# Kernel optimization log

Hardware: AMD Instinct MI355X
Metric: run time of the kernel (lower is better)

Reference implementation:

```python
import jax, jax.numpy as jnp
import numpy as np

ALPHA = 0.1
EPS = 1e-10

def setup_inputs() -> dict:
    key = jax.random.key(0)
    k1, k2 = jax.random.split(key)
    x = jax.random.normal(k1, (64, 8192, 128), dtype=jnp.float32)   # [B, N, D]
    pv = jax.random.uniform(k2, (64, 128), dtype=jnp.float32)        # [M, D] prototypes (torch.rand init)
    return {"x": x, "pv": pv}

def _cdist(x, pv):
    # Euclidean pairwise distance via GEMM form: [B,N,D] x [M,D] -> [B,N,M]
    x2 = jnp.sum(x * x, axis=-1, keepdims=True)          # [B,N,1]
    p2 = jnp.sum(pv * pv, axis=-1)                        # [M]
    xp = jnp.einsum('bnd,md->bnm', x, pv)                 # [B,N,M]
    return jnp.sqrt(jnp.maximum(x2 + p2 - 2.0 * xp, 0.0))

def reference(x, pv):
    dist = _cdist(x, pv)                                  # [B,N,M]
    min_dist = jnp.min(dist, axis=1)                      # [B,M] closest patch per prototype
    min_pos = jnp.argmin(dist, axis=1)                    # [B,M]
    # pick, per batch, the patch position of the globally closest prototype (no-grad in original)
    idx = jnp.argmin(min_dist, axis=1)                    # [B]
    min_pos = min_pos[jnp.arange(min_pos.shape[0]), idx]  # [B]
    max_sim = jnp.exp(EPS - ALPHA * min_dist)             # [B,M]
    return (max_sim, min_pos)
```

## Files before the change

### kernel.cpp

```cpp
#include <hip/hip_runtime.h>
#include <cfloat>
#include <cmath>

#define B_ 64
#define N_ 8192
#define D_ 128
#define M_ 64
#define CROWS 64
#define NCHUNK 4
#define BROWS (CROWS*NCHUNK)
#define NBLK (N_/BROWS)
#define ALPHA_ 0.1f
#define EPS_ 1e-10f

typedef __attribute__((ext_vector_type(4))) float f32x4;
typedef __attribute__((ext_vector_type(8))) short bf16x8;
typedef __attribute__((ext_vector_type(4))) short s16x4;

static __device__ __forceinline__ short f2bf(float f) {
    unsigned u = __float_as_uint(f);
    u += 0x7fff + ((u >> 16) & 1);
    return (short)(u >> 16);
}
static __device__ __forceinline__ float bf2f(short s) {
    return __uint_as_float(((unsigned)(unsigned short)s) << 16);
}

__global__ __launch_bounds__(256, 2)
void protomin_mfma(const float* __restrict__ x, const float* __restrict__ pv,
                   float* __restrict__ wsv, int* __restrict__ wsa) {
    __shared__ short xhi[2][CROWS * D_];
    __shared__ short xlo[2][CROWS * D_];
    __shared__ float x2s[2][CROWS];
    __shared__ float redv[4][M_];
    __shared__ int   redp[4][M_];

    const int tid = threadIdx.x;
    const int w   = tid >> 6;
    const int l   = tid & 63;
    const int lm  = l & 15, lg = l >> 4;
    const int bid = blockIdx.x;
    const int b   = bid >> 5;
    const int nbase = (bid & 31) * BROWS;

    const float* xblk = x + ((size_t)b * N_ + nbase) * D_;

    f32x4 nv[8];
    {
        const f32x4* src = (const f32x4*)xblk;
#pragma unroll
        for (int i = 0; i < 8; ++i) nv[i] = src[(w * 8 + i) * 64 + l];
    }

    bf16x8 Bh[4][4], Bl[4][4];
#pragma unroll
    for (int mt = 0; mt < 4; ++mt) {
#pragma unroll
        for (int kt = 0; kt < 4; ++kt) {
            const float* p = pv + (mt * 16 + lm) * D_ + kt * 32 + lg * 8;
            f32x4 p0 = *(const f32x4*)p;
            f32x4 p1 = *(const f32x4*)(p + 4);
#pragma unroll
            for (int j = 0; j < 4; ++j) {
                short h = f2bf(p0[j]);
                Bh[mt][kt][j] = h;
                Bl[mt][kt][j] = f2bf(p0[j] - bf2f(h));
            }
#pragma unroll
            for (int j = 0; j < 4; ++j) {
                short h = f2bf(p1[j]);
                Bh[mt][kt][4 + j] = h;
                Bl[mt][kt][4 + j] = f2bf(p1[j] - bf2f(h));
            }
        }
    }

    auto stage = [&](int buf) {
#pragma unroll
        for (int i = 0; i < 8; ++i) {
            int seg = w * 8 + i;
            int row = seg * 2 + (l >> 5);
            int ks  = (l & 31) * 4;
            f32x4 v = nv[i];
            float s = v[0] * v[0];
            s = fmaf(v[1], v[1], s); s = fmaf(v[2], v[2], s); s = fmaf(v[3], v[3], s);
            s += __shfl_xor(s, 1);  s += __shfl_xor(s, 2);  s += __shfl_xor(s, 4);
            s += __shfl_xor(s, 8);  s += __shfl_xor(s, 16);
            if ((l & 31) == 0) x2s[buf][row] = s;
            s16x4 hv, lv;
#pragma unroll
            for (int j = 0; j < 4; ++j) {
                short h = f2bf(v[j]);
                hv[j] = h;
                lv[j] = f2bf(v[j] - bf2f(h));
            }
            int sidx = row * D_ + (ks ^ ((row & 7) << 3));
            *(s16x4*)&xhi[buf][sidx] = hv;
            *(s16x4*)&xlo[buf][sidx] = lv;
        }
    };

    float bv[4]; int bp[4];
#pragma unroll
    for (int mt = 0; mt < 4; ++mt) { bv[mt] = FLT_MAX; bp[mt] = 0; }

    stage(0);
    __syncthreads();

    for (int c = 0; c < NCHUNK; ++c) {
        const int cur = c & 1;
        if (c + 1 < NCHUNK) {
            const f32x4* src = (const f32x4*)(xblk + (size_t)(c + 1) * CROWS * D_);
#pragma unroll
            for (int i = 0; i < 8; ++i) nv[i] = src[(w * 8 + i) * 64 + l];
        }

        f32x4 acc[4] = {};
        const int arow  = w * 16 + lm;
        const int abase = arow * D_;
        const int aswz  = (arow & 7) << 3;
#pragma unroll
        for (int kt = 0; kt < 4; ++kt) {
            int koff = (kt * 32 + lg * 8) ^ aswz;
            bf16x8 ah = *(const bf16x8*)&xhi[cur][abase + koff];
            bf16x8 al = *(const bf16x8*)&xlo[cur][abase + koff];
#pragma unroll
            for (int mt = 0; mt < 4; ++mt) {
                acc[mt] = __builtin_amdgcn_mfma_f32_16x16x32_bf16(ah, Bh[mt][kt], acc[mt], 0, 0, 0);
                acc[mt] = __builtin_amdgcn_mfma_f32_16x16x32_bf16(al, Bh[mt][kt], acc[mt], 0, 0, 0);
                acc[mt] = __builtin_amdgcn_mfma_f32_16x16x32_bf16(ah, Bl[mt][kt], acc[mt], 0, 0, 0);
                acc[mt] = __builtin_amdgcn_mfma_f32_16x16x32_bf16(al, Bl[mt][kt], acc[mt], 0, 0, 0);
            }
        }

        float x2v[4];
        const int rbase = w * 16 + lg * 4;
#pragma unroll
        for (int r = 0; r < 4; ++r) x2v[r] = x2s[cur][rbase + r];
        const int npos0 = nbase + c * CROWS + rbase;
#pragma unroll
        for (int mt = 0; mt < 4; ++mt) {
#pragma unroll
            for (int r = 0; r < 4; ++r) {
                float cand = fmaf(-2.f, acc[mt][r], x2v[r]);
                if (cand < bv[mt]) { bv[mt] = cand; bp[mt] = npos0 + r; }
            }
        }

        if (c + 1 < NCHUNK) stage(cur ^ 1);
        __syncthreads();
    }

#pragma unroll
    for (int mt = 0; mt < 4; ++mt) {
        float v = bv[mt]; int p = bp[mt];
#pragma unroll
        for (int off = 16; off <= 32; off <<= 1) {
            float ov = __shfl_xor(v, off);
            int   op = __shfl_xor(p, off);
            if (ov < v || (ov == v && op < p)) { v = ov; p = op; }
        }
        if (l < 16) { redv[w][mt * 16 + l] = v; redp[w][mt * 16 + l] = p; }
    }
    __syncthreads();

    if (tid < M_) {
        float v = redv[0][tid]; int p = redp[0][tid];
#pragma unroll
        for (int w2 = 1; w2 < 4; ++w2) {
            float ov = redv[w2][tid]; int op = redp[w2][tid];
            if (ov < v || (ov == v && op < p)) { v = ov; p = op; }
        }
        wsv[(size_t)bid * M_ + tid] = v;
        wsa[(size_t)bid * M_ + tid] = p;
    }
}

__global__ void finalize_kernel(const float* __restrict__ wsv,
                                const int* __restrict__ wsa,
                                const float* __restrict__ pv,
                                float* __restrict__ out) {
    const int b = blockIdx.x;
    const int m = threadIdx.x;

    float p2 = 0.f;
    const f32x4* pp = (const f32x4*)(pv + m * D_);
#pragma unroll 8
    for (int j = 0; j < 32; ++j) {
        f32x4 v = pp[j];
        p2 = fmaf(v[0], v[0], p2); p2 = fmaf(v[1], v[1], p2);
        p2 = fmaf(v[2], v[2], p2); p2 = fmaf(v[3], v[3], p2);
    }

    float v = FLT_MAX; int p = 0;
    for (int bc = 0; bc < NBLK; ++bc) {
        size_t idx = ((size_t)(b * NBLK + bc)) * M_ + m;
        float nv2 = wsv[idx]; int np = wsa[idx];
        if (nv2 < v || (nv2 == v && np < p)) { v = nv2; p = np; }
    }
    float dist = sqrtf(fmaxf(v + p2, 0.f));
    out[b * M_ + m] = expf(EPS_ - ALPHA_ * dist);

    __shared__ float sv[M_];
    __shared__ int   sa[M_];
    sv[m] = dist; sa[m] = p;
    __syncthreads();
    if (m == 0) {
        float best = FLT_MAX; int bpos = 0;
        for (int k = 0; k < M_; ++k)
            if (sv[k] < best) { best = sv[k]; bpos = sa[k]; }
        out[B_ * M_ + b] = (float)bpos;
    }
}

extern "C" void kernel_launch(void* const* d_in, const int* in_sizes, int n_in,
                              void* d_out, int out_size, void* d_ws, size_t ws_size,
                              hipStream_t stream) {
    const float* x  = (const float*)d_in[0];
    const float* pv = (const float*)d_in[1];
    float* out = (float*)d_out;

    float* wsv = (float*)d_ws;
    int*   wsa = (int*)((char*)d_ws + (size_t)B_ * NBLK * M_ * sizeof(float));

    hipLaunchKernelGGL(protomin_mfma, dim3(B_ * NBLK), dim3(256), 0, stream,
                       x, pv, wsv, wsa);
    hipLaunchKernelGGL(finalize_kernel, dim3(B_), dim3(M_), 0, stream,
                       wsv, wsa, pv, out);
}
```

Baseline: 449.5 us.

## Split warps into a 2x2 row/prototype tile grid to halve B-fragment registers

Each wave now owns 32 rows by 32 prototypes instead of 16 rows by 64 prototypes. The bf16 hi/lo prototype fragments held in registers drop by half, which cuts register pressure and may allow more occupancy. In exchange each wave loads twice as many A fragments from LDS per k-step. The cross-wave reduction is reduced to combining two row halves.

```diff
diff --git a/kernel.cpp b/kernel.cpp
--- a/kernel.cpp
+++ b/kernel.cpp
@@ -32,13 +32,15 @@
     __shared__ short xhi[2][CROWS * D_];
     __shared__ short xlo[2][CROWS * D_];
     __shared__ float x2s[2][CROWS];
-    __shared__ float redv[4][M_];
-    __shared__ int   redp[4][M_];
+    __shared__ float redv[2][M_];
+    __shared__ int   redp[2][M_];
 
     const int tid = threadIdx.x;
     const int w   = tid >> 6;
     const int l   = tid & 63;
     const int lm  = l & 15, lg = l >> 4;
+    const int wr  = w & 1;
+    const int wm  = w >> 1;
     const int bid = blockIdx.x;
     const int b   = bid >> 5;
     const int nbase = (bid & 31) * BROWS;
@@ -52,25 +54,25 @@
         for (int i = 0; i < 8; ++i) nv[i] = src[(w * 8 + i) * 64 + l];
     }
 
-    bf16x8 Bh[4][4], Bl[4][4];
-#pragma unroll
-    for (int mt = 0; mt < 4; ++mt) {
+    bf16x8 Bh[2][4], Bl[2][4];
+#pragma unroll
+    for (int mti = 0; mti < 2; ++mti) {
 #pragma unroll
         for (int kt = 0; kt < 4; ++kt) {
-            const float* p = pv + (mt * 16 + lm) * D_ + kt * 32 + lg * 8;
+            const float* p = pv + (wm * 32 + mti * 16 + lm) * D_ + kt * 32 + lg * 8;
             f32x4 p0 = *(const f32x4*)p;
             f32x4 p1 = *(const f32x4*)(p + 4);
 #pragma unroll
             for (int j = 0; j < 4; ++j) {
                 short h = f2bf(p0[j]);
-                Bh[mt][kt][j] = h;
-                Bl[mt][kt][j] = f2bf(p0[j] - bf2f(h));
+                Bh[mti][kt][j] = h;
+                Bl[mti][kt][j] = f2bf(p0[j] - bf2f(h));
             }
 #pragma unroll
             for (int j = 0; j < 4; ++j) {
                 short h = f2bf(p1[j]);
-                Bh[mt][kt][4 + j] = h;
-                Bl[mt][kt][4 + j] = f2bf(p1[j] - bf2f(h));
+                Bh[mti][kt][4 + j] = h;
+                Bl[mti][kt][4 + j] = f2bf(p1[j] - bf2f(h));
             }
         }
     }
@@ -100,9 +102,9 @@
         }
     };
 
-    float bv[4]; int bp[4];
-#pragma unroll
-    for (int mt = 0; mt < 4; ++mt) { bv[mt] = FLT_MAX; bp[mt] = 0; }
+    float bv[2]; int bp[2];
+#pragma unroll
+    for (int mti = 0; mti < 2; ++mti) { bv[mti] = FLT_MAX; bp[mti] = 0; }
 
     stage(0);
     __syncthreads();
@@ -115,35 +117,43 @@
             for (int i = 0; i < 8; ++i) nv[i] = src[(w * 8 + i) * 64 + l];
         }
 
-        f32x4 acc[4] = {};
-        const int arow  = w * 16 + lm;
-        const int abase = arow * D_;
-        const int aswz  = (arow & 7) << 3;
+        f32x4 acc[2][2] = {};
 #pragma unroll
         for (int kt = 0; kt < 4; ++kt) {
-            int koff = (kt * 32 + lg * 8) ^ aswz;
-            bf16x8 ah = *(const bf16x8*)&xhi[cur][abase + koff];
-            bf16x8 al = *(const bf16x8*)&xlo[cur][abase + koff];
-#pragma unroll
-            for (int mt = 0; mt < 4; ++mt) {
-                acc[mt] = __builtin_amdgcn_mfma_f32_16x16x32_bf16(ah, Bh[mt][kt], acc[mt], 0, 0, 0);
-                acc[mt] = __builtin_amdgcn_mfma_f32_16x16x32_bf16(al, Bh[mt][kt], acc[mt], 0, 0, 0);
-                acc[mt] = __builtin_amdgcn_mfma_f32_16x16x32_bf16(ah, Bl[mt][kt], acc[mt], 0, 0, 0);
-                acc[mt] = __builtin_amdgcn_mfma_f32_16x16x32_bf16(al, Bl[mt][kt], acc[mt], 0, 0, 0);
-            }
-        }
-
-        float x2v[4];
-        const int rbase = w * 16 + lg * 4;
-#pragma unroll
-        for (int r = 0; r < 4; ++r) x2v[r] = x2s[cur][rbase + r];
-        const int npos0 = nbase + c * CROWS + rbase;
-#pragma unroll
-        for (int mt = 0; mt < 4; ++mt) {
-#pragma unroll
-            for (int r = 0; r < 4; ++r) {
-                float cand = fmaf(-2.f, acc[mt][r], x2v[r]);
-                if (cand < bv[mt]) { bv[mt] = cand; bp[mt] = npos0 + r; }
+            bf16x8 ah[2], al[2];
+#pragma unroll
+            for (int rt = 0; rt < 2; ++rt) {
+                int arow = wr * 32 + rt * 16 + lm;
+                int koff = (kt * 32 + lg * 8) ^ ((arow & 7) << 3);
+                ah[rt] = *(const bf16x8*)&xhi[cur][arow * D_ + koff];
+                al[rt] = *(const bf16x8*)&xlo[cur][arow * D_ + koff];
+            }
+#pragma unroll
+            for (int rt = 0; rt < 2; ++rt) {
+#pragma unroll
+                for (int mti = 0; mti < 2; ++mti) {
+                    acc[rt][mti] = __builtin_amdgcn_mfma_f32_16x16x32_bf16(ah[rt], Bh[mti][kt], acc[rt][mti], 0, 0, 0);
+                    acc[rt][mti] = __builtin_amdgcn_mfma_f32_16x16x32_bf16(al[rt], Bh[mti][kt], acc[rt][mti], 0, 0, 0);
+                    acc[rt][mti] = __builtin_amdgcn_mfma_f32_16x16x32_bf16(ah[rt], Bl[mti][kt], acc[rt][mti], 0, 0, 0);
+                    acc[rt][mti] = __builtin_amdgcn_mfma_f32_16x16x32_bf16(al[rt], Bl[mti][kt], acc[rt][mti], 0, 0, 0);
+                }
+            }
+        }
+
+#pragma unroll
+        for (int rt = 0; rt < 2; ++rt) {
+            const int rbase = wr * 32 + rt * 16 + lg * 4;
+            float x2v[4];
+#pragma unroll
+            for (int r = 0; r < 4; ++r) x2v[r] = x2s[cur][rbase + r];
+            const int npos0 = nbase + c * CROWS + rbase;
+#pragma unroll
+            for (int mti = 0; mti < 2; ++mti) {
+#pragma unroll
+                for (int r = 0; r < 4; ++r) {
+                    float cand = fmaf(-2.f, acc[rt][mti][r], x2v[r]);
+                    if (cand < bv[mti]) { bv[mti] = cand; bp[mti] = npos0 + r; }
+                }
             }
         }
 
@@ -152,25 +162,23 @@
     }
 
 #pragma unroll
-    for (int mt = 0; mt < 4; ++mt) {
-        float v = bv[mt]; int p = bp[mt];
+    for (int mti = 0; mti < 2; ++mti) {
+        float v = bv[mti]; int p = bp[mti];
 #pragma unroll
         for (int off = 16; off <= 32; off <<= 1) {
             float ov = __shfl_xor(v, off);
             int   op = __shfl_xor(p, off);
             if (ov < v || (ov == v && op < p)) { v = ov; p = op; }
         }
-        if (l < 16) { redv[w][mt * 16 + l] = v; redp[w][mt * 16 + l] = p; }
+        if (l < 16) { redv[wr][wm * 32 + mti * 16 + l] = v;
+                      redp[wr][wm * 32 + mti * 16 + l] = p; }
     }
     __syncthreads();
 
     if (tid < M_) {
         float v = redv[0][tid]; int p = redp[0][tid];
-#pragma unroll
-        for (int w2 = 1; w2 < 4; ++w2) {
-            float ov = redv[w2][tid]; int op = redp[w2][tid];
-            if (ov < v || (ov == v && op < p)) { v = ov; p = op; }
-        }
+        float ov = redv[1][tid]; int op = redp[1][tid];
+        if (ov < v || (ov == v && op < p)) { v = ov; p = op; }
         wsv[(size_t)bid * M_ + tid] = v;
         wsa[(size_t)bid * M_ + tid] = p;
     }
```

New measurement: 377.3 us. -16.1%, faster.
